# Kernel tuning notes

Measured on AMD Instinct MI355X. Metric: run time of the kernel, lower is better.

The kernel has to match this reference:

```python
import jax, jax.numpy as jnp
import numpy as np

IN_FEATURES = 4096
OUT_FEATURES = 2048
N_GROUPS = 16  # group size = IN_FEATURES // N_GROUPS = 256


def setup_inputs() -> dict:
    key = jax.random.key(0)
    k1, k2, k3, k4 = jax.random.split(key, 4)
    x = jax.random.normal(k1, (8, 64, IN_FEATURES), dtype=jnp.float32)
    # uint8 quantized weights, stored [out, in] as in the torch module
    qweight = jax.random.randint(k2, (OUT_FEATURES, IN_FEATURES), 0, 256).astype(jnp.uint8)
    # per-(out-channel, group) dequant scale and offset; scale ~ (max-min)/255 of rand weights
    qrange = jax.random.uniform(k3, (OUT_FEATURES, N_GROUPS), dtype=jnp.float32) * (2.0 / 255.0)
    qmin = -jax.random.uniform(k4, (OUT_FEATURES, N_GROUPS), dtype=jnp.float32)
    return {"x": x, "qweight": qweight, "qrange": qrange, "qmin": qmin}


def reference(x, qweight, qrange, qmin):
    # out[b,s,o] = sum_i x[b,s,i] * (q[o,i]*qrange[o,g(i)] + qmin[o,g(i)])
    B, S, IN = x.shape
    OUT, G = qrange.shape
    gs = IN // G
    xg = x.reshape(B, S, G, gs)                     # [B,S,G,gs]
    qg = qweight.reshape(OUT, G, gs).astype(x.dtype)  # [O,G,gs]
    # fused per-group dequant matmul: scale folded into the contraction
    out = jnp.einsum('bsgi,ogi,og->bso', xg, qg, qrange)
    # offset term: qmin[o,g] * sum_i_in_group x[b,s,i]
    out = out + jnp.einsum('bsg,og->bso', xg.sum(axis=-1), qmin)
    return out
```

## Files before the change

kernel.cpp:

```cpp
#include <hip/hip_runtime.h>
#include <hip/hip_bf16.h>


#define M_T 512
#define N_T 2048
#define K_T 4096
#define NGRP 16
#define BM 128
#define BN 128
#define BK 64
#define OUT_ELEMS (M_T * N_T)

typedef __attribute__((ext_vector_type(8))) short mfrag_t;
typedef __attribute__((ext_vector_type(8))) unsigned short u16x8;
typedef __attribute__((ext_vector_type(4))) float f32x4;

__device__ __forceinline__ unsigned short f2bf(float f) {
  union { __hip_bfloat16 h; unsigned short u; } c;
  c.h = __float2bfloat16(f);
  return c.u;
}

template <int KSPLIT, bool ATOMIC, bool XCDSWZ>
__global__ __launch_bounds__(512, 4) void dq_gemm_kernel(
    const float* __restrict__ x, const int* __restrict__ qw,
    const float* __restrict__ qrange, const float* __restrict__ qmin,
    float* __restrict__ dst) {
  constexpr int KC = K_T / KSPLIT;
  constexpr int NTC = KC / BK;

  __shared__ __align__(16) unsigned short As[BM * BK];
  __shared__ __align__(16) unsigned short Bs[BN * BK];

  const int tid = threadIdx.x;
  int xt, yt, kc;
  if (XCDSWZ) {
    const int b = blockIdx.x;
    kc = b & 7;
    const int slot = b >> 3;
    xt = slot & 15;
    yt = slot >> 4;
  } else {
    const int b = blockIdx.x;
    xt = b & 15;
    yt = (b >> 4) & 3;
    kc = b >> 6;
  }
  const int n0 = xt * BN;
  const int m0 = yt * BM;
  const int kbase = kc * KC;

  const int srow = tid >> 2;
  const int sseg = tid & 3;

  const float* xp = x + (size_t)(m0 + srow) * K_T + kbase + sseg * 16;
  const int* qp = qw + (size_t)(n0 + srow) * K_T + kbase + sseg * 16;
  const float* qrp = qrange + (size_t)(n0 + srow) * NGRP;
  const float* qmp = qmin + (size_t)(n0 + srow) * NGRP;

  const int lane = tid & 63;
  const int wv = tid >> 6;
  const int wm = (wv >> 2) * 64;
  const int wn = (wv & 3) * 32;
  const int lr = lane & 15;
  const int lq = lane >> 4;

  float4 av[4];
  int4 qv[4];
  float sc, mn;

  {
    const float* a = xp;
    av[0] = *(const float4*)(a + 0);
    av[1] = *(const float4*)(a + 4);
    av[2] = *(const float4*)(a + 8);
    av[3] = *(const float4*)(a + 12);
    const int4* q = (const int4*)qp;
    qv[0] = q[0]; qv[1] = q[1]; qv[2] = q[2]; qv[3] = q[3];
    sc = qrp[kc * (KC / 256)];
    mn = qmp[kc * (KC / 256)];
  }

  f32x4 acc[4][2] = {};

  const int rx7 = srow & 7;
  const int abase = srow * BK;
  const int wslot0 = ((sseg * 2) ^ rx7) << 3;
  const int wslot1 = ((sseg * 2 + 1) ^ rx7) << 3;
  const int rxl = lr & 7;

  for (int t = 0; t < NTC; ++t) {
    if (t > 0) __syncthreads();

    {
      u16x8 pa0, pa1, pb0, pb1;
      pa0[0] = f2bf(av[0].x); pa0[1] = f2bf(av[0].y); pa0[2] = f2bf(av[0].z); pa0[3] = f2bf(av[0].w);
      pa0[4] = f2bf(av[1].x); pa0[5] = f2bf(av[1].y); pa0[6] = f2bf(av[1].z); pa0[7] = f2bf(av[1].w);
      pa1[0] = f2bf(av[2].x); pa1[1] = f2bf(av[2].y); pa1[2] = f2bf(av[2].z); pa1[3] = f2bf(av[2].w);
      pa1[4] = f2bf(av[3].x); pa1[5] = f2bf(av[3].y); pa1[6] = f2bf(av[3].z); pa1[7] = f2bf(av[3].w);
      pb0[0] = f2bf((float)qv[0].x * sc + mn); pb0[1] = f2bf((float)qv[0].y * sc + mn);
      pb0[2] = f2bf((float)qv[0].z * sc + mn); pb0[3] = f2bf((float)qv[0].w * sc + mn);
      pb0[4] = f2bf((float)qv[1].x * sc + mn); pb0[5] = f2bf((float)qv[1].y * sc + mn);
      pb0[6] = f2bf((float)qv[1].z * sc + mn); pb0[7] = f2bf((float)qv[1].w * sc + mn);
      pb1[0] = f2bf((float)qv[2].x * sc + mn); pb1[1] = f2bf((float)qv[2].y * sc + mn);
      pb1[2] = f2bf((float)qv[2].z * sc + mn); pb1[3] = f2bf((float)qv[2].w * sc + mn);
      pb1[4] = f2bf((float)qv[3].x * sc + mn); pb1[5] = f2bf((float)qv[3].y * sc + mn);
      pb1[6] = f2bf((float)qv[3].z * sc + mn); pb1[7] = f2bf((float)qv[3].w * sc + mn);
      *(u16x8*)&As[abase + wslot0] = pa0;
      *(u16x8*)&As[abase + wslot1] = pa1;
      *(u16x8*)&Bs[abase + wslot0] = pb0;
      *(u16x8*)&Bs[abase + wslot1] = pb1;
    }

    if (t + 1 < NTC) {
      const float* a = xp + (size_t)(t + 1) * BK;
      av[0] = *(const float4*)(a + 0);
      av[1] = *(const float4*)(a + 4);
      av[2] = *(const float4*)(a + 8);
      av[3] = *(const float4*)(a + 12);
      const int4* q = (const int4*)(qp + (size_t)(t + 1) * BK);
      qv[0] = q[0]; qv[1] = q[1]; qv[2] = q[2]; qv[3] = q[3];
      const int g = kc * (KC / 256) + ((t + 1) >> 2);
      sc = qrp[g];
      mn = qmp[g];
    }

    __syncthreads();

#pragma unroll
    for (int kk = 0; kk < 2; ++kk) {
      const int so = ((kk * 4 + lq) ^ rxl) << 3;
      mfrag_t af[4], bf[2];
#pragma unroll
      for (int fm = 0; fm < 4; ++fm)
        af[fm] = *(const mfrag_t*)&As[(wm + fm * 16 + lr) * BK + so];
#pragma unroll
      for (int fn = 0; fn < 2; ++fn)
        bf[fn] = *(const mfrag_t*)&Bs[(wn + fn * 16 + lr) * BK + so];
#pragma unroll
      for (int fm = 0; fm < 4; ++fm)
#pragma unroll
        for (int fn = 0; fn < 2; ++fn)
          acc[fm][fn] = __builtin_amdgcn_mfma_f32_16x16x32_bf16(af[fm], bf[fn], acc[fm][fn], 0, 0, 0);
    }
  }

  float* base = ATOMIC ? dst : dst + (size_t)kc * OUT_ELEMS;
#pragma unroll
  for (int fm = 0; fm < 4; ++fm) {
#pragma unroll
    for (int fn = 0; fn < 2; ++fn) {
      const int r0 = m0 + wm + fm * 16 + lq * 4;
      const int c = n0 + wn + fn * 16 + lr;
      float* op = base + (size_t)r0 * N_T + c;
      if (ATOMIC) {
        atomicAdd(&op[0 * (size_t)N_T], acc[fm][fn][0]);
        atomicAdd(&op[1 * (size_t)N_T], acc[fm][fn][1]);
        atomicAdd(&op[2 * (size_t)N_T], acc[fm][fn][2]);
        atomicAdd(&op[3 * (size_t)N_T], acc[fm][fn][3]);
      } else {
        op[0 * (size_t)N_T] = acc[fm][fn][0];
        op[1 * (size_t)N_T] = acc[fm][fn][1];
        op[2 * (size_t)N_T] = acc[fm][fn][2];
        op[3 * (size_t)N_T] = acc[fm][fn][3];
      }
    }
  }
}

template <int KSPLIT>
__global__ __launch_bounds__(256) void reduce_kernel(const float* __restrict__ ws,
                                                     float* __restrict__ out) {
  const int i4 = blockIdx.x * 256 + threadIdx.x;
  const size_t base = (size_t)i4 * 4;
  float4 a = *(const float4*)(ws + base);
#pragma unroll
  for (int s = 1; s < KSPLIT; ++s) {
    float4 b = *(const float4*)(ws + (size_t)s * OUT_ELEMS + base);
    a.x += b.x; a.y += b.y; a.z += b.z; a.w += b.w;
  }
  *(float4*)(out + base) = a;
}

extern "C" void kernel_launch(void* const* d_in, const int* in_sizes, int n_in,
                              void* d_out, int out_size, void* d_ws, size_t ws_size,
                              hipStream_t stream) {
  const float* x = (const float*)d_in[0];
  const int* qw = (const int*)d_in[1];
  const float* qr = (const float*)d_in[2];
  const float* qm = (const float*)d_in[3];
  float* out = (float*)d_out;
  float* ws = (float*)d_ws;

  constexpr int KS = 8;
  const size_t need = (size_t)KS * OUT_ELEMS * sizeof(float);
  if (ws_size >= need) {
    const int nblk = (N_T / BN) * (M_T / BM) * KS;
    dq_gemm_kernel<KS, false, true><<<nblk, dim3(512, 1, 1), 0, stream>>>(x, qw, qr, qm, ws);
    reduce_kernel<KS><<<OUT_ELEMS / 4 / 256, 256, 0, stream>>>(ws, out);
  } else {
    hipMemsetAsync(out, 0, (size_t)OUT_ELEMS * sizeof(float), stream);
    const int nblk = (N_T / BN) * (M_T / BM) * 4;
    dq_gemm_kernel<4, true, false><<<nblk, dim3(512, 1, 1), 0, stream>>>(x, qw, qr, qm, out);
  }
}
```

Measured before the change: 35.45 us.

## Pre-pack dequantized weights and activations to bf16 in a separate kernel

Result: no change. 35.55 us (+0.3%).

```diff
diff --git a/kernel.cpp b/kernel.cpp
--- a/kernel.cpp
+++ b/kernel.cpp
@@ -10,6 +10,8 @@
 #define BN 128
 #define BK 64
 #define OUT_ELEMS (M_T * N_T)
+#define W_ELEMS (N_T * K_T)
+#define X_ELEMS (M_T * K_T)
 
 typedef __attribute__((ext_vector_type(8))) short mfrag_t;
 typedef __attribute__((ext_vector_type(8))) unsigned short u16x8;
@@ -21,10 +23,41 @@
   return c.u;
 }
 
-template <int KSPLIT, bool ATOMIC, bool XCDSWZ>
-__global__ __launch_bounds__(512, 4) void dq_gemm_kernel(
+__global__ __launch_bounds__(256) void pack_kernel(
     const float* __restrict__ x, const int* __restrict__ qw,
     const float* __restrict__ qrange, const float* __restrict__ qmin,
+    unsigned short* __restrict__ wsW, unsigned short* __restrict__ wsX) {
+  const int bid = blockIdx.x;
+  const int tid = threadIdx.x;
+  if (bid < (W_ELEMS / 8) / 256) {
+    const int gidx = bid * 256 + tid;
+    const int o = gidx >> 9;
+    const int k8 = gidx & 511;
+    const int g = k8 >> 5;
+    const float sc = qrange[o * NGRP + g];
+    const float mn = qmin[o * NGRP + g];
+    const int4* q = (const int4*)(qw + ((size_t)o << 12) + (k8 << 3));
+    const int4 q0 = q[0], q1 = q[1];
+    u16x8 p;
+    p[0] = f2bf((float)q0.x * sc + mn); p[1] = f2bf((float)q0.y * sc + mn);
+    p[2] = f2bf((float)q0.z * sc + mn); p[3] = f2bf((float)q0.w * sc + mn);
+    p[4] = f2bf((float)q1.x * sc + mn); p[5] = f2bf((float)q1.y * sc + mn);
+    p[6] = f2bf((float)q1.z * sc + mn); p[7] = f2bf((float)q1.w * sc + mn);
+    *(u16x8*)(wsW + ((size_t)gidx << 3)) = p;
+  } else {
+    const int gidx = (bid - (W_ELEMS / 8) / 256) * 256 + tid;
+    const float4* a = (const float4*)(x + ((size_t)gidx << 3));
+    const float4 a0 = a[0], a1 = a[1];
+    u16x8 p;
+    p[0] = f2bf(a0.x); p[1] = f2bf(a0.y); p[2] = f2bf(a0.z); p[3] = f2bf(a0.w);
+    p[4] = f2bf(a1.x); p[5] = f2bf(a1.y); p[6] = f2bf(a1.z); p[7] = f2bf(a1.w);
+    *(u16x8*)(wsX + ((size_t)gidx << 3)) = p;
+  }
+}
+
+template <int KSPLIT, bool XCDSWZ>
+__global__ __launch_bounds__(512, 4) void dq_gemm_kernel(
+    const unsigned short* __restrict__ wsX, const unsigned short* __restrict__ wsW,
     float* __restrict__ dst) {
   constexpr int KC = K_T / KSPLIT;
   constexpr int NTC = KC / BK;
@@ -53,10 +86,8 @@
   const int srow = tid >> 2;
   const int sseg = tid & 3;
 
-  const float* xp = x + (size_t)(m0 + srow) * K_T + kbase + sseg * 16;
-  const int* qp = qw + (size_t)(n0 + srow) * K_T + kbase + sseg * 16;
-  const float* qrp = qrange + (size_t)(n0 + srow) * NGRP;
-  const float* qmp = qmin + (size_t)(n0 + srow) * NGRP;
+  const unsigned short* ap = wsX + (size_t)(m0 + srow) * K_T + kbase + sseg * 16;
+  const unsigned short* bp = wsW + (size_t)(n0 + srow) * K_T + kbase + sseg * 16;
 
   const int lane = tid & 63;
   const int wv = tid >> 6;
@@ -65,64 +96,38 @@
   const int lr = lane & 15;
   const int lq = lane >> 4;
 
-  float4 av[4];
-  int4 qv[4];
-  float sc, mn;
-
-  {
-    const float* a = xp;
-    av[0] = *(const float4*)(a + 0);
-    av[1] = *(const float4*)(a + 4);
-    av[2] = *(const float4*)(a + 8);
-    av[3] = *(const float4*)(a + 12);
-    const int4* q = (const int4*)qp;
-    qv[0] = q[0]; qv[1] = q[1]; qv[2] = q[2]; qv[3] = q[3];
-    sc = qrp[kc * (KC / 256)];
-    mn = qmp[kc * (KC / 256)];
-  }
-
-  f32x4 acc[4][2] = {};
-
   const int rx7 = srow & 7;
   const int abase = srow * BK;
   const int wslot0 = ((sseg * 2) ^ rx7) << 3;
   const int wslot1 = ((sseg * 2 + 1) ^ rx7) << 3;
   const int rxl = lr & 7;
 
+  u16x8 av0, av1, bv0, bv1;
+
+  {
+    av0 = *(const u16x8*)(ap);
+    av1 = *(const u16x8*)(ap + 8);
+    bv0 = *(const u16x8*)(bp);
+    bv1 = *(const u16x8*)(bp + 8);
+  }
+
+  f32x4 acc[4][2] = {};
+
   for (int t = 0; t < NTC; ++t) {
     if (t > 0) __syncthreads();
 
-    {
-      u16x8 pa0, pa1, pb0, pb1;
-      pa0[0] = f2bf(av[0].x); pa0[1] = f2bf(av[0].y); pa0[2] = f2bf(av[0].z); pa0[3] = f2bf(av[0].w);
-      pa0[4] = f2bf(av[1].x); pa0[5] = f2bf(av[1].y); pa0[6] = f2bf(av[1].z); pa0[7] = f2bf(av[1].w);
-      pa1[0] = f2bf(av[2].x); pa1[1] = f2bf(av[2].y); pa1[2] = f2bf(av[2].z); pa1[3] = f2bf(av[2].w);
-      pa1[4] = f2bf(av[3].x); pa1[5] = f2bf(av[3].y); pa1[6] = f2bf(av[3].z); pa1[7] = f2bf(av[3].w);
-      pb0[0] = f2bf((float)qv[0].x * sc + mn); pb0[1] = f2bf((float)qv[0].y * sc + mn);
-      pb0[2] = f2bf((float)qv[0].z * sc + mn); pb0[3] = f2bf((float)qv[0].w * sc + mn);
-      pb0[4] = f2bf((float)qv[1].x * sc + mn); pb0[5] = f2bf((float)qv[1].y * sc + mn);
-      pb0[6] = f2bf((float)qv[1].z * sc + mn); pb0[7] = f2bf((float)qv[1].w * sc + mn);
-      pb1[0] = f2bf((float)qv[2].x * sc + mn); pb1[1] = f2bf((float)qv[2].y * sc + mn);
-      pb1[2] = f2bf((float)qv[2].z * sc + mn); pb1[3] = f2bf((float)qv[2].w * sc + mn);
-      pb1[4] = f2bf((float)qv[3].x * sc + mn); pb1[5] = f2bf((float)qv[3].y * sc + mn);
-      pb1[6] = f2bf((float)qv[3].z * sc + mn); pb1[7] = f2bf((float)qv[3].w * sc + mn);
-      *(u16x8*)&As[abase + wslot0] = pa0;
-      *(u16x8*)&As[abase + wslot1] = pa1;
-      *(u16x8*)&Bs[abase + wslot0] = pb0;
-      *(u16x8*)&Bs[abase + wslot1] = pb1;
-    }
+    *(u16x8*)&As[abase + wslot0] = av0;
+    *(u16x8*)&As[abase + wslot1] = av1;
+    *(u16x8*)&Bs[abase + wslot0] = bv0;
+    *(u16x8*)&Bs[abase + wslot1] = bv1;
 
     if (t + 1 < NTC) {
-      const float* a = xp + (size_t)(t + 1) * BK;
-      av[0] = *(const float4*)(a + 0);
-      av[1] = *(const float4*)(a + 4);
-      av[2] = *(const float4*)(a + 8);
-      av[3] = *(const float4*)(a + 12);
-      const int4* q = (const int4*)(qp + (size_t)(t + 1) * BK);
-      qv[0] = q[0]; qv[1] = q[1]; qv[2] = q[2]; qv[3] = q[3];
-      const int g = kc * (KC / 256) + ((t + 1) >> 2);
-      sc = qrp[g];
-      mn = qmp[g];
+      const unsigned short* a_ = ap + (size_t)(t + 1) * BK;
+      const unsigned short* b_ = bp + (size_t)(t + 1) * BK;
+      av0 = *(const u16x8*)(a_);
+      av1 = *(const u16x8*)(a_ + 8);
+      bv0 = *(const u16x8*)(b_);
+      bv1 = *(const u16x8*)(b_ + 8);
     }
 
     __syncthreads();
@@ -145,7 +150,7 @@
     }
   }
 
-  float* base = ATOMIC ? dst : dst + (size_t)kc * OUT_ELEMS;
+  float* base = dst + (size_t)kc * OUT_ELEMS;
 #pragma unroll
   for (int fm = 0; fm < 4; ++fm) {
 #pragma unroll
@@ -153,17 +158,10 @@
       const int r0 = m0 + wm + fm * 16 + lq * 4;
       const int c = n0 + wn + fn * 16 + lr;
       float* op = base + (size_t)r0 * N_T + c;
-      if (ATOMIC) {
-        atomicAdd(&op[0 * (size_t)N_T], acc[fm][fn][0]);
-        atomicAdd(&op[1 * (size_t)N_T], acc[fm][fn][1]);
-        atomicAdd(&op[2 * (size_t)N_T], acc[fm][fn][2]);
-        atomicAdd(&op[3 * (size_t)N_T], acc[fm][fn][3]);
-      } else {
-        op[0 * (size_t)N_T] = acc[fm][fn][0];
-        op[1 * (size_t)N_T] = acc[fm][fn][1];
-        op[2 * (size_t)N_T] = acc[fm][fn][2];
-        op[3 * (size_t)N_T] = acc[fm][fn][3];
-      }
+      op[0 * (size_t)N_T] = acc[fm][fn][0];
+      op[1 * (size_t)N_T] = acc[fm][fn][1];
+      op[2 * (size_t)N_T] = acc[fm][fn][2];
+      op[3 * (size_t)N_T] = acc[fm][fn][3];
     }
   }
 }
@@ -180,6 +178,25 @@
     a.x += b.x; a.y += b.y; a.z += b.z; a.w += b.w;
   }
   *(float4*)(out + base) = a;
+}
+
+__global__ void naive_kernel(const float* __restrict__ x, const int* __restrict__ qw,
+                             const float* __restrict__ qrange, const float* __restrict__ qmin,
+                             float* __restrict__ out) {
+  const int idx = blockIdx.x * 256 + threadIdx.x;
+  if (idx >= OUT_ELEMS) return;
+  const int m = idx / N_T, n = idx % N_T;
+  float s = 0.f;
+  for (int g = 0; g < NGRP; ++g) {
+    const float sc = qrange[n * NGRP + g], mn = qmin[n * NGRP + g];
+    float d = 0.f, xs = 0.f;
+    for (int k = g * 256; k < (g + 1) * 256; ++k) {
+      d += x[(size_t)m * K_T + k] * (float)qw[(size_t)n * K_T + k];
+      xs += x[(size_t)m * K_T + k];
+    }
+    s += d * sc + xs * mn;
+  }
+  out[idx] = s;
 }
 
 extern "C" void kernel_launch(void* const* d_in, const int* in_sizes, int n_in,
@@ -190,17 +207,20 @@
   const float* qr = (const float*)d_in[2];
   const float* qm = (const float*)d_in[3];
   float* out = (float*)d_out;
-  float* ws = (float*)d_ws;
 
   constexpr int KS = 8;
-  const size_t need = (size_t)KS * OUT_ELEMS * sizeof(float);
+  unsigned short* wsW = (unsigned short*)d_ws;
+  unsigned short* wsX = wsW + W_ELEMS;
+  float* partials = (float*)(wsX + X_ELEMS);
+  const size_t need = (size_t)W_ELEMS * 2 + (size_t)X_ELEMS * 2 +
+                      (size_t)KS * OUT_ELEMS * sizeof(float);
   if (ws_size >= need) {
+    const int packblk = (W_ELEMS / 8) / 256 + (X_ELEMS / 8) / 256;
+    pack_kernel<<<packblk, 256, 0, stream>>>(x, qw, qr, qm, wsW, wsX);
     const int nblk = (N_T / BN) * (M_T / BM) * KS;
-    dq_gemm_kernel<KS, false, true><<<nblk, dim3(512, 1, 1), 0, stream>>>(x, qw, qr, qm, ws);
-    reduce_kernel<KS><<<OUT_ELEMS / 4 / 256, 256, 0, stream>>>(ws, out);
+    dq_gemm_kernel<KS, true><<<nblk, dim3(512, 1, 1), 0, stream>>>(wsX, wsW, partials);
+    reduce_kernel<KS><<<OUT_ELEMS / 4 / 256, 256, 0, stream>>>(partials, out);
   } else {
-    hipMemsetAsync(out, 0, (size_t)OUT_ELEMS * sizeof(float), stream);
-    const int nblk = (N_T / BN) * (M_T / BM) * 4;
-    dq_gemm_kernel<4, true, false><<<nblk, dim3(512, 1, 1), 0, stream>>>(x, qw, qr, qm, out);
-  }
-}
+    naive_kernel<<<(OUT_ELEMS + 255) / 256, 256, 0, stream>>>(x, qw, qr, qm, out);
+  }
+}
```
